# Kernel tuning notes

Hardware: AMD Instinct MI355X
Metric: run time of the kernel (lower is better)

## Reference

```python
import jax, jax.numpy as jnp
import numpy as np
from jax import lax

B, T, SLEN = 65536, 512, 12

def setup_inputs() -> dict:
    key = jax.random.key(0)
    k0, k1, k2 = jax.random.split(key, 3)
    series = jax.random.normal(k0, (B, T), dtype=jnp.float32)
    series_shifts = jax.random.randint(k1, (B,), 0, SLEN)
    init_season = jax.random.uniform(k2, (SLEN,), dtype=jnp.float32)
    return {
        'series': series,
        'series_shifts': series_shifts,
        'alpha': jnp.asarray(0.1, jnp.float32),
        'beta': jnp.asarray(0.1, jnp.float32),
        'gamma': jnp.asarray(0.1, jnp.float32),
        'init_season': init_season,
        'init_trend': jnp.asarray(0.1, jnp.float32),
        'n_preds': 0,  # only runnable value (original code indexes series[:, i] for all i)
    }


def reference(series, series_shifts, alpha, beta, gamma, init_season, init_trend, n_preds):
    # series: (B, T) float32; series_shifts: (B,) int roll amounts
    b, t = series.shape
    slen = init_season.shape[0]
    # Per-batch rolled initial seasonals, as in torch.roll(init_season, shift)
    rolled = jax.vmap(lambda r: jnp.roll(init_season, r))(series_shifts)  # (B, slen)
    # In the original code seasonals[i % slen] always reads the INITIAL rolled
    # seasonal (appended gamma-updates live at indices >= slen and are never read),
    # so the seasonal sequence is fully determined up-front.
    seas = rolled[:, jnp.arange(t) % slen]  # (B, T)

    smooth0 = series[:, 0]                              # (B,)
    trend0 = jnp.full((b,), init_trend, series.dtype)   # (B,)
    res0 = smooth0 + trend0                             # i == 0 output (no seasonal)

    def step(carry, x):
        smooth, trend = carry
        y, season_prev = x  # series[:, i], seasonal at i % slen
        smooth_new = alpha * (y - season_prev) + (1.0 - alpha) * (smooth + trend)
        trend_new = beta * (smooth_new - smooth) + (1.0 - beta) * trend
        res = smooth_new + trend_new + season_prev
        return (smooth_new, trend_new), res

    xs = (series[:, 1:].T, seas[:, 1:].T)  # (T-1, B) each
    _, res_rest = lax.scan(step, (smooth0, trend0), xs)  # (T-1, B)
    result = jnp.concatenate([res0[None, :], res_rest], axis=0).T  # (B, T)
    # n_preds == 0: original returns result[:, -0:] == full series
    return result if n_preds == 0 else result[:, -n_preds:]
```

## Files before the change

### kernel.cpp

```cpp
#include <hip/hip_runtime.h>

#define NB 65536
#define NT 512
#define SLEN 12
#define BLOCK 256
#define ROWS 8
#define CHUNKS 32
#define CLEN 16
#define CSTR 20
#define ROWSTR (CHUNKS * CSTR)
#define YSZ (ROWS * ROWSTR)

__global__ __launch_bounds__(BLOCK) void holtwinters_kernel(
    const float* __restrict__ series,
    const int*   __restrict__ shifts,
    const float* __restrict__ alpha_p,
    const float* __restrict__ beta_p,
    const float* __restrict__ init_season,
    const float* __restrict__ trend0_p,
    float*       __restrict__ out)
{
    __shared__ __align__(16) float  y[YSZ];
    __shared__ float2 endst[ROWS * CHUNKS];
    __shared__ float2 sarr [ROWS * CHUNKS];
    __shared__ float2 u[CLEN + 1];
    __shared__ float  Mm[4];
    __shared__ float  ss[SLEN];

    const int t    = threadIdx.x;
    const int row0 = blockIdx.x * ROWS;

    const float alpha  = alpha_p[0];
    const float beta   = beta_p[0];
    const float oma    = 1.0f - alpha;
    const float omb    = 1.0f - beta;
    const float trend0 = trend0_p[0];

    if (t < SLEN) ss[t] = init_season[t];

    if (t == 0) {
        const float a00 = oma, a01 = oma;
        const float a10 = -alpha * beta, a11 = beta * oma + omb;
        float p0 = 1.0f, p1 = 1.0f;
        for (int j = 1; j <= CLEN; ++j) {
            const float q0 = p0 * a00 + p1 * a10;
            const float q1 = p0 * a01 + p1 * a11;
            p0 = q0; p1 = q1;
            u[j] = make_float2(p0, p1);
        }
        float m00 = a00, m01 = a01, m10 = a10, m11 = a11;
        for (int sq = 0; sq < 4; ++sq) {
            const float n00 = m00 * m00 + m01 * m10;
            const float n01 = m00 * m01 + m01 * m11;
            const float n10 = m10 * m00 + m11 * m10;
            const float n11 = m10 * m01 + m11 * m11;
            m00 = n00; m01 = n01; m10 = n10; m11 = n11;
        }
        Mm[0] = m00; Mm[1] = m01; Mm[2] = m10; Mm[3] = m11;
    }

    {
        const float4* __restrict__ src = (const float4*)(series + (size_t)row0 * NT);
        #pragma unroll
        for (int i = 0; i < 4; ++i) {
            const int g   = t + i * BLOCK;
            const int r   = g >> 7;
            const int col = (g & 127) * 4;
            const int c   = col >> 4, k = col & 15;
            const float4 v = src[g];
            *(float4*)&y[r * ROWSTR + c * CSTR + k] = v;
        }
    }
    __syncthreads();

    const int r = t >> 5;
    const int c = t & 31;
    const int shift = shifts[row0 + r];
    int sidx = ((c * CLEN - shift) % SLEN + SLEN) % SLEN;

    float o[CLEN];
    float smooth = 0.0f, trend = 0.0f;
    {
        const float* yb = &y[r * ROWSTR + c * CSTR];
        #pragma unroll
        for (int q = 0; q < 4; ++q) {
            const float4 yv = *(const float4*)(yb + 4 * q);
            const float ya[4] = {yv.x, yv.y, yv.z, yv.w};
            #pragma unroll
            for (int kk = 0; kk < 4; ++kk) {
                const int k = 4 * q + kk;
                const float s = ss[sidx];
                sidx = (sidx + 1 == SLEN) ? 0 : sidx + 1;
                const float yy = ya[kk];
                if (c == 0 && k == 0) {
                    smooth = yy;
                    trend  = trend0;
                    o[0]   = smooth + trend;
                } else {
                    const float st = smooth + trend;
                    const float sm = alpha * (yy - s) + oma * st;
                    trend  = beta * (sm - smooth) + omb * trend;
                    smooth = sm;
                    o[k]   = sm + trend + s;
                }
            }
        }
    }
    endst[t] = make_float2(smooth, trend);
    __syncthreads();

    if (c == 0) {
        const float m00 = Mm[0], m01 = Mm[1], m10 = Mm[2], m11 = Mm[3];
        float2 e0 = endst[r * CHUNKS + 0];
        float Sx = e0.x, Sy = e0.y;
        sarr[r * CHUNKS + 1] = make_float2(Sx, Sy);
        for (int cc = 2; cc < CHUNKS; ++cc) {
            const float2 rr = endst[r * CHUNKS + cc - 1];
            const float nx = m00 * Sx + m01 * Sy + rr.x;
            const float ny = m10 * Sx + m11 * Sy + rr.y;
            Sx = nx; Sy = ny;
            sarr[r * CHUNKS + cc] = make_float2(Sx, Sy);
        }
    }
    __syncthreads();

    if (c != 0) {
        const float2 S = sarr[r * CHUNKS + c];
        #pragma unroll
        for (int k = 0; k < CLEN; ++k) {
            const float2 uk = u[k + 1];
            o[k] += uk.x * S.x + uk.y * S.y;
        }
    }
    {
        float* yb = &y[r * ROWSTR + c * CSTR];
        #pragma unroll
        for (int q = 0; q < 4; ++q)
            *(float4*)(yb + 4 * q) =
                make_float4(o[4*q], o[4*q+1], o[4*q+2], o[4*q+3]);
    }
    __syncthreads();

    {
        float4* __restrict__ dst = (float4*)(out + (size_t)row0 * NT);
        #pragma unroll
        for (int i = 0; i < 4; ++i) {
            const int g   = t + i * BLOCK;
            const int rr  = g >> 7;
            const int col = (g & 127) * 4;
            const int cc  = col >> 4, kk = col & 15;
            dst[g] = *(const float4*)&y[rr * ROWSTR + cc * CSTR + kk];
        }
    }
}

extern "C" void kernel_launch(void* const* d_in, const int* in_sizes, int n_in,
                              void* d_out, int out_size, void* d_ws, size_t ws_size,
                              hipStream_t stream) {
    const float* series      = (const float*)d_in[0];
    const int*   shifts      = (const int*)  d_in[1];
    const float* alpha       = (const float*)d_in[2];
    const float* beta        = (const float*)d_in[3];
    const float* init_season = (const float*)d_in[5];
    const float* init_trend  = (const float*)d_in[6];
    float*       out         = (float*)d_out;

    dim3 block(BLOCK);
    dim3 grid(NB / ROWS);
    hipLaunchKernelGGL(holtwinters_kernel, grid, block, 0, stream,
                       series, shifts, alpha, beta, init_season, init_trend, out);
}
```

Measured before the change: 242.3 us.

## Replace serial chunk-carry scan with wave shuffle scan and direct global I/O

Swaps the serial per-row carry propagation done by one lane (31 dependent steps through shared memory) for a 5-step Kogge-Stone shuffle scan. It uses precomputed matrix powers M^(16·2^d) stored in shared memory. It also drops the shared-memory staging of input and output, so each thread loads and stores its own 16 contiguous floats directly. This removes most __syncthreads and LDS traffic. In exchange, global accesses become strided per thread (64B per lane), which is less coalesced than the previous float4 row-contiguous pattern.

```diff
diff --git a/kernel.cpp b/kernel.cpp
--- a/kernel.cpp
+++ b/kernel.cpp
@@ -1,15 +1,12 @@
 #include <hip/hip_runtime.h>
 
-#define NB 65536
-#define NT 512
-#define SLEN 12
+#define NB    65536
+#define NT    512
+#define SLEN  12
 #define BLOCK 256
-#define ROWS 8
+#define ROWS  8
 #define CHUNKS 32
-#define CLEN 16
-#define CSTR 20
-#define ROWSTR (CHUNKS * CSTR)
-#define YSZ (ROWS * ROWSTR)
+#define CLEN  16
 
 __global__ __launch_bounds__(BLOCK) void holtwinters_kernel(
     const float* __restrict__ series,
@@ -20,16 +17,11 @@
     const float* __restrict__ trend0_p,
     float*       __restrict__ out)
 {
-    __shared__ __align__(16) float  y[YSZ];
-    __shared__ float2 endst[ROWS * CHUNKS];
-    __shared__ float2 sarr [ROWS * CHUNKS];
+    __shared__ float  ss[SLEN];
     __shared__ float2 u[CLEN + 1];
-    __shared__ float  Mm[4];
-    __shared__ float  ss[SLEN];
+    __shared__ float4 Mp[5];
 
-    const int t    = threadIdx.x;
-    const int row0 = blockIdx.x * ROWS;
-
+    const int t = threadIdx.x;
     const float alpha  = alpha_p[0];
     const float beta   = beta_p[0];
     const float oma    = 1.0f - alpha;
@@ -37,7 +29,6 @@
     const float trend0 = trend0_p[0];
 
     if (t < SLEN) ss[t] = init_season[t];
-
     if (t == 0) {
         const float a00 = oma, a01 = oma;
         const float a10 = -alpha * beta, a11 = beta * oma + omb;
@@ -50,108 +41,83 @@
         }
         float m00 = a00, m01 = a01, m10 = a10, m11 = a11;
         for (int sq = 0; sq < 4; ++sq) {
-            const float n00 = m00 * m00 + m01 * m10;
-            const float n01 = m00 * m01 + m01 * m11;
-            const float n10 = m10 * m00 + m11 * m10;
-            const float n11 = m10 * m01 + m11 * m11;
+            const float n00 = m00*m00 + m01*m10;
+            const float n01 = m00*m01 + m01*m11;
+            const float n10 = m10*m00 + m11*m10;
+            const float n11 = m10*m01 + m11*m11;
             m00 = n00; m01 = n01; m10 = n10; m11 = n11;
         }
-        Mm[0] = m00; Mm[1] = m01; Mm[2] = m10; Mm[3] = m11;
-    }
-
-    {
-        const float4* __restrict__ src = (const float4*)(series + (size_t)row0 * NT);
-        #pragma unroll
-        for (int i = 0; i < 4; ++i) {
-            const int g   = t + i * BLOCK;
-            const int r   = g >> 7;
-            const int col = (g & 127) * 4;
-            const int c   = col >> 4, k = col & 15;
-            const float4 v = src[g];
-            *(float4*)&y[r * ROWSTR + c * CSTR + k] = v;
+        for (int d = 0; d < 5; ++d) {
+            Mp[d] = make_float4(m00, m01, m10, m11);
+            const float n00 = m00*m00 + m01*m10;
+            const float n01 = m00*m01 + m01*m11;
+            const float n10 = m10*m00 + m11*m10;
+            const float n11 = m10*m01 + m11*m11;
+            m00 = n00; m01 = n01; m10 = n10; m11 = n11;
         }
     }
     __syncthreads();
 
-    const int r = t >> 5;
-    const int c = t & 31;
-    const int shift = shifts[row0 + r];
+    const int r     = t >> 5;
+    const int c     = t & 31;
+    const int row   = blockIdx.x * ROWS + r;
+    const int shift = shifts[row];
     int sidx = ((c * CLEN - shift) % SLEN + SLEN) % SLEN;
 
+    const float* __restrict__ yb = series + (size_t)row * NT + c * CLEN;
     float o[CLEN];
+    *(float4*)&o[0]  = *(const float4*)(yb + 0);
+    *(float4*)&o[4]  = *(const float4*)(yb + 4);
+    *(float4*)&o[8]  = *(const float4*)(yb + 8);
+    *(float4*)&o[12] = *(const float4*)(yb + 12);
+
     float smooth = 0.0f, trend = 0.0f;
-    {
-        const float* yb = &y[r * ROWSTR + c * CSTR];
-        #pragma unroll
-        for (int q = 0; q < 4; ++q) {
-            const float4 yv = *(const float4*)(yb + 4 * q);
-            const float ya[4] = {yv.x, yv.y, yv.z, yv.w};
-            #pragma unroll
-            for (int kk = 0; kk < 4; ++kk) {
-                const int k = 4 * q + kk;
-                const float s = ss[sidx];
-                sidx = (sidx + 1 == SLEN) ? 0 : sidx + 1;
-                const float yy = ya[kk];
-                if (c == 0 && k == 0) {
-                    smooth = yy;
-                    trend  = trend0;
-                    o[0]   = smooth + trend;
-                } else {
-                    const float st = smooth + trend;
-                    const float sm = alpha * (yy - s) + oma * st;
-                    trend  = beta * (sm - smooth) + omb * trend;
-                    smooth = sm;
-                    o[k]   = sm + trend + s;
-                }
-            }
+    #pragma unroll
+    for (int k = 0; k < CLEN; ++k) {
+        const float s = ss[sidx];
+        sidx = (sidx + 1 == SLEN) ? 0 : sidx + 1;
+        const float yy = o[k];
+        if (c == 0 && k == 0) {
+            smooth = yy;
+            trend  = trend0;
+            o[0]   = smooth + trend;
+        } else {
+            const float st = smooth + trend;
+            const float sm = alpha * (yy - s) + oma * st;
+            trend  = beta * (sm - smooth) + omb * trend;
+            smooth = sm;
+            o[k]   = sm + trend + s;
         }
     }
-    endst[t] = make_float2(smooth, trend);
-    __syncthreads();
 
-    if (c == 0) {
-        const float m00 = Mm[0], m01 = Mm[1], m10 = Mm[2], m11 = Mm[3];
-        float2 e0 = endst[r * CHUNKS + 0];
-        float Sx = e0.x, Sy = e0.y;
-        sarr[r * CHUNKS + 1] = make_float2(Sx, Sy);
-        for (int cc = 2; cc < CHUNKS; ++cc) {
-            const float2 rr = endst[r * CHUNKS + cc - 1];
-            const float nx = m00 * Sx + m01 * Sy + rr.x;
-            const float ny = m10 * Sx + m11 * Sy + rr.y;
-            Sx = nx; Sy = ny;
-            sarr[r * CHUNKS + cc] = make_float2(Sx, Sy);
+    float Ex = smooth, Ey = trend;
+    #pragma unroll
+    for (int d = 0; d < 5; ++d) {
+        const float4 m  = Mp[d];
+        const int    dd = 1 << d;
+        const float gx = __shfl_up(Ex, dd, CHUNKS);
+        const float gy = __shfl_up(Ey, dd, CHUNKS);
+        if (c >= dd) {
+            Ex += m.x * gx + m.y * gy;
+            Ey += m.z * gx + m.w * gy;
         }
     }
-    __syncthreads();
+    const float Sx = __shfl_up(Ex, 1, CHUNKS);
+    const float Sy = __shfl_up(Ey, 1, CHUNKS);
 
     if (c != 0) {
-        const float2 S = sarr[r * CHUNKS + c];
         #pragma unroll
         for (int k = 0; k < CLEN; ++k) {
             const float2 uk = u[k + 1];
-            o[k] += uk.x * S.x + uk.y * S.y;
+            o[k] += uk.x * Sx + uk.y * Sy;
         }
     }
-    {
-        float* yb = &y[r * ROWSTR + c * CSTR];
-        #pragma unroll
-        for (int q = 0; q < 4; ++q)
-            *(float4*)(yb + 4 * q) =
-                make_float4(o[4*q], o[4*q+1], o[4*q+2], o[4*q+3]);
-    }
-    __syncthreads();
 
-    {
-        float4* __restrict__ dst = (float4*)(out + (size_t)row0 * NT);
-        #pragma unroll
-        for (int i = 0; i < 4; ++i) {
-            const int g   = t + i * BLOCK;
-            const int rr  = g >> 7;
-            const int col = (g & 127) * 4;
-            const int cc  = col >> 4, kk = col & 15;
-            dst[g] = *(const float4*)&y[rr * ROWSTR + cc * CSTR + kk];
-        }
-    }
+    float* __restrict__ ob = out + (size_t)row * NT + c * CLEN;
+    *(float4*)(ob + 0)  = *(float4*)&o[0];
+    *(float4*)(ob + 4)  = *(float4*)&o[4];
+    *(float4*)(ob + 8)  = *(float4*)&o[8];
+    *(float4*)(ob + 12) = *(float4*)&o[12];
 }
 
 extern "C" void kernel_launch(void* const* d_in, const int* in_sizes, int n_in,
```

Result: no change. 246.0 us (+1.5%).
